# Kernel optimization log

Hardware: AMD Instinct MI355X
Metric: run time of the kernel (lower is better)

## Reference

```python
import jax, jax.numpy as jnp
import numpy as np

N_EMBED = 1024
SEQ_LEN = 2048
BATCH = 4


def setup_inputs() -> dict:
    key = jax.random.key(0)
    ks = jax.random.split(key, 9)
    E = N_EMBED
    x = jax.random.normal(ks[0], (BATCH, SEQ_LEN, E), dtype=jnp.float32)
    s = 0.02
    return {
        "x": x,
        "Wq": jax.random.normal(ks[1], (E, E), dtype=jnp.float32) * s,
        "bq": jnp.zeros((E,), dtype=jnp.float32),
        "Wk": jax.random.normal(ks[2], (E, E), dtype=jnp.float32) * s,
        "bk": jnp.zeros((E,), dtype=jnp.float32),
        "Wv": jax.random.normal(ks[3], (E, E), dtype=jnp.float32) * s,
        "bv": jnp.zeros((E,), dtype=jnp.float32),
        "Wp": jax.random.normal(ks[4], (E, E), dtype=jnp.float32) * s,
        "bp": jnp.zeros((E,), dtype=jnp.float32),
    }


def reference(x, Wq, bq, Wk, bk, Wv, bv, Wp, bp):
    # x: [B, S, E]. Original torch code unpacks (B, C, N) = x.shape and
    # scales by sqrt(C) == sqrt(seq_len)  (a bug we faithfully replicate).
    B, S, E = x.shape
    q = jnp.einsum('bse,fe->bsf', x, Wq) + bq
    k = jnp.einsum('bse,fe->bsf', x, Wk) + bk
    v = jnp.einsum('bse,fe->bsf', x, Wv) + bv
    scale = 1.0 / jnp.sqrt(jnp.asarray(S, dtype=x.dtype))
    scores = jnp.einsum('bqe,bke->bqk', q, k) * scale  # [B, S, S]
    # NOTE: original calls masked_fill (non-inplace) and discards the result,
    # so NO causal mask is actually applied. Replicate that: plain softmax.
    w = jax.nn.softmax(scores, axis=-1)
    o = jnp.einsum('bqk,bke->bqe', w, v)
    out = jnp.einsum('bse,fe->bsf', o, Wp) + bp
    return out
```

## Files before the change

### kernel.cpp

```cpp
#include <hip/hip_runtime.h>


typedef __bf16 bf16x8 __attribute__((ext_vector_type(8)));
typedef float  f32x4  __attribute__((ext_vector_type(4)));
typedef unsigned short u16x8 __attribute__((ext_vector_type(8)));

__device__ __forceinline__ float bf2f(unsigned short u) {
  return __uint_as_float(((unsigned int)u) << 16);
}
__device__ __forceinline__ unsigned short f2bf(float f) {
  unsigned int u = __float_as_uint(f);
  return (unsigned short)((u + 0x7fffu + ((u >> 16) & 1u)) >> 16);
}
__device__ __forceinline__ void gload16(const void* g, void* l) {
  __builtin_amdgcn_global_load_lds(
      (const __attribute__((address_space(1))) void*)g,
      (__attribute__((address_space(3))) void*)l, 16, 0, 0);
}

__global__ __launch_bounds__(256) void cvt_str(
    const float* __restrict__ x, const float* __restrict__ wp,
    unsigned short* __restrict__ x_bf, unsigned short* __restrict__ wp_bf) {
  const float* s;
  unsigned short* d;
  int i;
  if (blockIdx.x < 4096) {
    s = x; d = x_bf; i = (blockIdx.x * 256 + threadIdx.x) * 8;
  } else {
    s = wp; d = wp_bf; i = ((blockIdx.x - 4096) * 256 + threadIdx.x) * 8;
  }
  f32x4 a = *(const f32x4*)(s + i);
  f32x4 b = *(const f32x4*)(s + i + 4);
  u16x8 o;
  o[0] = f2bf(a[0]); o[1] = f2bf(a[1]); o[2] = f2bf(a[2]); o[3] = f2bf(a[3]);
  o[4] = f2bf(b[0]); o[5] = f2bf(b[1]); o[6] = f2bf(b[2]); o[7] = f2bf(b[3]);
  *(u16x8*)(d + i) = o;
}

__global__ __launch_bounds__(256) void cvt_T(
    const float* __restrict__ wq, const float* __restrict__ wk,
    const float* __restrict__ wv, unsigned short* __restrict__ qt,
    unsigned short* __restrict__ kt, unsigned short* __restrict__ vt) {
  const float* in;
  unsigned short* out;
  int b = blockIdx.x;
  if (b < 256)      { in = wq; out = qt; }
  else if (b < 512) { in = wk; out = kt; b -= 256; }
  else              { in = wv; out = vt; b -= 512; }
  const int r0 = (b >> 4) * 64, c0 = (b & 15) * 64;
  __shared__ unsigned short t[64][72];
  const int tid = threadIdx.x;
  const int rr = tid >> 4;
  const int cc4 = (tid & 15) * 4;
#pragma unroll
  for (int p = 0; p < 4; ++p) {
    const int r = rr + p * 16;
    f32x4 v = *(const f32x4*)(in + (size_t)(r0 + r) * 1024 + c0 + cc4);
    t[cc4 + 0][r] = f2bf(v[0]);
    t[cc4 + 1][r] = f2bf(v[1]);
    t[cc4 + 2][r] = f2bf(v[2]);
    t[cc4 + 3][r] = f2bf(v[3]);
  }
  __syncthreads();
  const int wr_ = tid >> 3;
  const int wc8 = (tid & 7) * 8;
#pragma unroll
  for (int p = 0; p < 2; ++p) {
    const int c = wr_ + p * 32;
    u16x8 o;
#pragma unroll
    for (int j = 0; j < 8; ++j) o[j] = t[c][wc8 + j];
    *(u16x8*)(out + (size_t)(c0 + c) * 1024 + r0 + wc8) = o;
  }
}

__global__ __launch_bounds__(256) void cvec(
    const float* __restrict__ bq, const float* __restrict__ Wk,
    const float* __restrict__ Wp, const float* __restrict__ bv,
    float* __restrict__ c1, float* __restrict__ cv, float scale) {
  if (blockIdx.x < 4) {
    const int e = blockIdx.x * 256 + threadIdx.x;
    float acc = 0.f;
    for (int f = 0; f < 1024; ++f) acc += bq[f] * Wk[(size_t)f * 1024 + e];
    c1[e] = acc * scale;
  } else {
    const int e = blockIdx.x - 4;
    float acc = 0.f;
    for (int f = threadIdx.x; f < 1024; f += 256)
      acc += Wp[(size_t)e * 1024 + f] * bv[f];
#pragma unroll
    for (int i = 1; i < 64; i <<= 1) acc += __shfl_xor(acc, i, 64);
    __shared__ float red[4];
    if ((threadIdx.x & 63) == 0) red[threadIdx.x >> 6] = acc;
    __syncthreads();
    if (threadIdx.x == 0) cv[e] = red[0] + red[1] + red[2] + red[3];
  }
}

template <int EPI>
__device__ __forceinline__ void gemm_core(
    char* lds, int nwg, int base,
    const unsigned short* __restrict__ A, const unsigned short* __restrict__ B,
    void* __restrict__ C, const float* __restrict__ bias,
    const float* __restrict__ rowsum,
    int K, long long sA, long long sB, long long sC,
    int nbm, int nbn, int ldc, float scale) {
  char* ldsA = lds;
  char* ldsB = lds + 98304;

  int id = (int)blockIdx.x - base;
  id = (id & 7) * (nwg >> 3) + (id >> 3);
  const int nbmn = nbm * nbn;
  const int bz = id / nbmn;
  const int rem = id - bz * nbmn;
  const int bm = rem / nbn;
  const int bn = rem - bm * nbn;
  const int gm0 = bm * 256, gn0 = bn * 128;

  const unsigned short* Ag = A + (size_t)bz * sA;
  const unsigned short* Bg = B + (size_t)bz * sB;

  const int tid = threadIdx.x;
  const int w = tid >> 6, l = tid & 63;
  const int wr = w >> 1, wc = w & 1;
  const int lr = l & 15;
  const int lk16 = (l >> 4) * 16;
  const int swz = (lr & 7) << 4;

  const int srow = tid >> 3;
  const int sbo  = ((tid & 7) * 16) ^ ((srow & 7) << 4);
  const int sdst = tid * 16;

#define STG_A(region, ktile)                                                   \
  do {                                                                         \
    const char* _b = (const char*)(Ag + (size_t)(gm0 + srow) * K) +            \
                     (size_t)(ktile) * 128 + sbo;                              \
    const size_t _rk = (size_t)64 * K * 2;                                     \
    gload16(_b,           (region) + sdst);                                    \
    gload16(_b + _rk,     (region) + 8192 + sdst);                             \
    gload16(_b + 2 * _rk, (region) + 16384 + sdst);                            \
    gload16(_b + 3 * _rk, (region) + 24576 + sdst);                            \
  } while (0)
#define STG_B(region, ktile)                                                   \
  do {                                                                         \
    const char* _b = (const char*)(Bg + (size_t)(gn0 + srow) * K) +            \
                     (size_t)(ktile) * 128 + sbo;                              \
    const size_t _rk = (size_t)64 * K * 2;                                     \
    gload16(_b,       (region) + sdst);                                        \
    gload16(_b + _rk, (region) + 8192 + sdst);                                 \
  } while (0)

#define RD_A(dst, m, kh)                                                       \
  dst = *(const bf16x8*)(Abuf + (wr * 64 + (m) * 16 + lr) * 128 +              \
                         ((lk16 + (kh) * 64) ^ swz))
#define RD_B(dst, n, kh)                                                       \
  dst = *(const bf16x8*)(Bbuf + (wc * 64 + (n) * 16 + lr) * 128 +              \
                         ((lk16 + (kh) * 64) ^ swz))

#define LGKM_PIN()                                          \
  asm volatile("s_waitcnt lgkmcnt(0)" ::: "memory");        \
  __builtin_amdgcn_sched_barrier(0)

  f32x4 acc[4][4];
#pragma unroll
  for (int i = 0; i < 4; ++i)
#pragma unroll
    for (int j = 0; j < 4; ++j) acc[i][j] = (f32x4){0.f, 0.f, 0.f, 0.f};

  const int nt = K >> 6;

  STG_B(ldsB, 0); STG_A(ldsA, 0);
  if (nt > 1) { STG_B(ldsB + 16384, 1); STG_A(ldsA + 32768, 1); }
  if (nt > 1) { asm volatile("s_waitcnt vmcnt(6)" ::: "memory"); }
  else        { asm volatile("s_waitcnt vmcnt(0)" ::: "memory"); }
  __builtin_amdgcn_s_barrier();

  int cur = 0;
  for (int t = 0; t < nt; ++t) {
    char* Abuf = ldsA + cur * 32768;
    char* Bbuf = ldsB + cur * 16384;
    const int nx2 = (cur + 2 >= 3) ? cur - 1 : cur + 2;
    const bool pf = (t + 2 < nt);

    bf16x8 af[4], bfr[4];
#pragma unroll
    for (int m = 0; m < 4; ++m) RD_A(af[m], m, 0);
#pragma unroll
    for (int n = 0; n < 4; ++n) RD_B(bfr[n], n, 0);
    if (pf) STG_B(ldsB + nx2 * 16384, t + 2);
    __builtin_amdgcn_s_barrier();
    LGKM_PIN();
    __builtin_amdgcn_s_setprio(1);
#pragma unroll
    for (int m = 0; m < 4; ++m)
#pragma unroll
      for (int n = 0; n < 4; ++n)
        acc[m][n] = __builtin_amdgcn_mfma_f32_16x16x32_bf16(af[m], bfr[n],
                                                            acc[m][n], 0, 0, 0);
    __builtin_amdgcn_s_setprio(0);
    __builtin_amdgcn_s_barrier();

#pragma unroll
    for (int m = 0; m < 4; ++m) RD_A(af[m], m, 1);
#pragma unroll
    for (int n = 0; n < 4; ++n) RD_B(bfr[n], n, 1);
    if (pf) STG_A(ldsA + nx2 * 32768, t + 2);
    __builtin_amdgcn_s_barrier();
    LGKM_PIN();
    __builtin_amdgcn_s_setprio(1);
#pragma unroll
    for (int m = 0; m < 4; ++m)
#pragma unroll
      for (int n = 0; n < 4; ++n)
        acc[m][n] = __builtin_amdgcn_mfma_f32_16x16x32_bf16(af[m], bfr[n],
                                                            acc[m][n], 0, 0, 0);
    __builtin_amdgcn_s_setprio(0);
    if (pf)              { asm volatile("s_waitcnt vmcnt(6)" ::: "memory"); }
    else if (t + 1 < nt) { asm volatile("s_waitcnt vmcnt(0)" ::: "memory"); }
    __builtin_amdgcn_s_barrier();

    cur = (cur + 1 >= 3) ? 0 : cur + 1;
  }

  const int cr = (l >> 4) * 4;
  const int cc = l & 15;
#pragma unroll
  for (int m = 0; m < 4; ++m) {
    const int row = gm0 + wr * 64 + m * 16 + cr;
    if constexpr (EPI == 3) {
      const float* rs = rowsum + bz * 2048 + row;
      const f32x4 rv = *(const f32x4*)rs;
      f32x4 inv;
#pragma unroll
      for (int j = 0; j < 4; ++j) inv[j] = 1.0f / rv[j];
      float* Cp = (float*)C + (size_t)bz * sC;
#pragma unroll
      for (int n = 0; n < 4; ++n) {
        const int col = gn0 + wc * 64 + n * 16 + cc;
        const float b = bias[col];
        f32x4 a = acc[m][n];
#pragma unroll
        for (int j = 0; j < 4; ++j)
          Cp[(size_t)(row + j) * ldc + col] = a[j] * inv[j] + b;
      }
    } else {
      unsigned short* Cp = (unsigned short*)C + (size_t)bz * sC;
#pragma unroll
      for (int n = 0; n < 4; ++n) {
        const int col = gn0 + wc * 64 + n * 16 + cc;
        f32x4 a = acc[m][n];
#pragma unroll
        for (int j = 0; j < 4; ++j) {
          float v;
          if constexpr (EPI == 1)      v = a[j] * scale;
          else if constexpr (EPI == 4) v = a[j] + bias[row + j];
          else                         v = a[j] + bias[col];
          Cp[(size_t)(row + j) * ldc + col] = f2bf(v);
        }
      }
    }
  }
#undef STG_A
#undef STG_B
#undef RD_A
#undef RD_B
#undef LGKM_PIN
}

__global__ __launch_bounds__(512) void gweights(
    const unsigned short* WkT, const unsigned short* WqT,
    const unsigned short* Wp, const unsigned short* WvT,
    unsigned short* HT, unsigned short* G, float scale) {
  __shared__ char lds[147456];
  if (blockIdx.x < 32)
    gemm_core<1>(lds, 32, 0, WkT, WqT, HT, nullptr, nullptr,
                 1024, 0, 0, 0, 4, 8, 1024, scale);
  else
    gemm_core<1>(lds, 32, 32, Wp, WvT, G, nullptr, nullptr,
                 1024, 0, 0, 0, 4, 8, 1024, 1.0f);
}
__global__ __launch_bounds__(512) void gr(
    const unsigned short* x, const unsigned short* HT, unsigned short* R,
    const float* c1) {
  __shared__ char lds[147456];
  gemm_core<5>(lds, 256, 0, x, HT, R, c1, nullptr,
               1024, 0, 0, 0, 32, 8, 1024, 0.f);
}
__global__ __launch_bounds__(512) void gvwt(
    const unsigned short* G, const unsigned short* x, unsigned short* VWt,
    const float* cv) {
  __shared__ char lds[147456];
  gemm_core<4>(lds, 256, 0, G, x, VWt, cv, nullptr,
               1024, 0, 2097152, 2097152, 4, 16, 2048, 0.f);
}
__global__ __launch_bounds__(512) void gout(
    const unsigned short* E, const unsigned short* VWt, float* out,
    const float* bp, const float* rowsum) {
  __shared__ char lds[147456];
  gemm_core<3>(lds, 256, 0, E, VWt, out, bp, rowsum,
               2048, 4194304, 2097152, 2097152, 8, 8, 1024, 0.f);
}

__global__ __launch_bounds__(512) void gsco8(
    const unsigned short* __restrict__ A, const unsigned short* __restrict__ B,
    unsigned short* __restrict__ C, float* __restrict__ rowsum,
    int K, long long sA, long long sB, long long sC, int nbm, int nbn) {
  __shared__ char lds[131072];
  char* ldsA = lds;
  char* ldsB = lds + 65536;

  const int nwg = (int)gridDim.x;
  int id = (int)blockIdx.x;
  id = (id & 7) * (nwg >> 3) + (id >> 3);
  const int nbmn = nbm * nbn;
  const int bz = id / nbmn;
  const int rem = id - bz * nbmn;
  const int bm = rem / nbn;
  const int bn = rem - bm * nbn;
  const int gm0 = bm * 256, gn0 = bn * 256;

  const unsigned short* Ag = A + (size_t)bz * sA;
  const unsigned short* Bg = B + (size_t)bz * sB;

  const int tid = threadIdx.x;
  const int w = tid >> 6, l = tid & 63;
  const int wr = w >> 2, wc = w & 3;
  const int lr = l & 15;
  const int lk16 = (l >> 4) * 16;
  const int swz = (lr & 7) << 4;

  const int srow0 = (tid * 16) >> 7;
  const int srow1 = srow0 + 64;
  const int sbo   = ((tid * 16) & 127) ^ ((srow0 & 7) << 4);
  const int sdst0 = tid * 16;
  const int sdst1 = tid * 16 + 8192;

#define STAGE(gbase, grow0, region, ktile)                                     \
  do {                                                                         \
    const char* _s0 =                                                          \
        (const char*)((gbase) + (size_t)((grow0) + srow0) * K) +               \
        (ktile) * 128 + sbo;                                                   \
    const char* _s1 =                                                          \
        (const char*)((gbase) + (size_t)((grow0) + srow1) * K) +               \
        (ktile) * 128 + sbo;                                                   \
    gload16(_s0, (region) + sdst0);                                            \
    gload16(_s1, (region) + sdst1);                                            \
  } while (0)

#define RDA(dst, m, kh) \
  dst = *(const bf16x8*)(Areg + ((m) * 16 + lr) * 128 + ((lk16 + (kh) * 64) ^ swz))
#define RDB(dst, n, kh) \
  dst = *(const bf16x8*)(Breg + (((wc & 1) * 64 + (n) * 16 + lr) * 128) + ((lk16 + (kh) * 64) ^ swz))

  f32x4 acc[8][4];
#pragma unroll
  for (int i = 0; i < 8; ++i)
#pragma unroll
    for (int j = 0; j < 4; ++j) acc[i][j] = (f32x4){0.f, 0.f, 0.f, 0.f};

  bf16x8 af[4][2], bf_[4][2];

#define MM(mi, ai, n)                                                          \
  acc[mi][n] = __builtin_amdgcn_mfma_f32_16x16x32_bf16(af[ai][0], bf_[n][0],   \
                                                       acc[mi][n], 0, 0, 0);   \
  acc[mi][n] = __builtin_amdgcn_mfma_f32_16x16x32_bf16(af[ai][1], bf_[n][1],   \
                                                       acc[mi][n], 0, 0, 0)

#define LGKM_PIN()                                          \
  asm volatile("s_waitcnt lgkmcnt(0)" ::: "memory");        \
  __builtin_amdgcn_sched_barrier(0)

  const int nt = K >> 6;

  STAGE(Bg, gn0,       ldsB + 0,     0);
  STAGE(Bg, gn0 + 128, ldsB + 16384, 0);
  STAGE(Ag, gm0,       ldsA + 0,     0);
  STAGE(Ag, gm0 + 128, ldsA + 16384, 0);
  STAGE(Bg, gn0,       ldsB + 32768,         1);
  STAGE(Bg, gn0 + 128, ldsB + 32768 + 16384, 1);
  STAGE(Ag, gm0,       ldsA + 32768,         1);
  asm volatile("s_waitcnt vmcnt(6)" ::: "memory");
  __builtin_amdgcn_s_barrier();

  for (int t = 0; t < nt; ++t) {
    const int cur = t & 1;
    char* Areg  = ldsA + cur * 32768 + wr * 16384;
    char* Breg  = ldsB + cur * 32768 + (wc >> 1) * 16384;
    char* Anext = ldsA + (cur ^ 1) * 32768;
    char* Acur2 = ldsA + cur * 32768;
    char* Bcur2 = ldsB + cur * 32768;

#pragma unroll
    for (int m = 0; m < 4; ++m) { RDA(af[m][0], m, 0); RDA(af[m][1], m, 1); }
#pragma unroll
    for (int n = 0; n < 2; ++n) { RDB(bf_[n][0], n, 0); RDB(bf_[n][1], n, 1); }
    if (wc < 2) {
#pragma unroll
      for (int n = 2; n < 4; ++n) { RDB(bf_[n][0], n, 0); RDB(bf_[n][1], n, 1); }
    }
    if (t + 1 < nt) STAGE(Ag, gm0 + 128, Anext + 16384, t + 1);
    __builtin_amdgcn_s_barrier();
    LGKM_PIN();
    __builtin_amdgcn_s_setprio(1);
    MM(0, 0, 0); MM(0, 0, 1); MM(1, 1, 0); MM(1, 1, 1);
    MM(2, 2, 0); MM(2, 2, 1); MM(3, 3, 0); MM(3, 3, 1);
    __builtin_amdgcn_s_setprio(0);
    __builtin_amdgcn_s_barrier();

    if (wc >= 2) {
#pragma unroll
      for (int n = 2; n < 4; ++n) { RDB(bf_[n][0], n, 0); RDB(bf_[n][1], n, 1); }
    }
    if (t + 2 < nt) STAGE(Bg, gn0, Bcur2, t + 2);
    __builtin_amdgcn_s_barrier();
    LGKM_PIN();
    __builtin_amdgcn_s_setprio(1);
    MM(0, 0, 2); MM(0, 0, 3); MM(1, 1, 2); MM(1, 1, 3);
    MM(2, 2, 2); MM(2, 2, 3); MM(3, 3, 2); MM(3, 3, 3);
    __builtin_amdgcn_s_setprio(0);
    __builtin_amdgcn_s_barrier();

#pragma unroll
    for (int m = 0; m < 4; ++m) { RDA(af[m][0], m + 4, 0); RDA(af[m][1], m + 4, 1); }
    if (t + 2 < nt) STAGE(Bg, gn0 + 128, Bcur2 + 16384, t + 2);
    __builtin_amdgcn_s_barrier();
    LGKM_PIN();
    __builtin_amdgcn_s_setprio(1);
    MM(4, 0, 0); MM(4, 0, 1); MM(5, 1, 0); MM(5, 1, 1);
    MM(6, 2, 0); MM(6, 2, 1); MM(7, 3, 0); MM(7, 3, 1);
    __builtin_amdgcn_s_setprio(0);
    __builtin_amdgcn_s_barrier();

    if (t + 2 < nt) STAGE(Ag, gm0, Acur2, t + 2);
    __builtin_amdgcn_s_barrier();
    __builtin_amdgcn_s_setprio(1);
    MM(4, 0, 2); MM(4, 0, 3); MM(5, 1, 2); MM(5, 1, 3);
    MM(6, 2, 2); MM(6, 2, 3); MM(7, 3, 2); MM(7, 3, 3);
    __builtin_amdgcn_s_setprio(0);
    if (t + 2 < nt) {
      asm volatile("s_waitcnt vmcnt(6)" ::: "memory");
    } else {
      asm volatile("s_waitcnt vmcnt(0)" ::: "memory");
    }
    __builtin_amdgcn_s_barrier();
  }

  const int cr = (l >> 4) * 4;
  const int cc = l & 15;
  unsigned short* Cp = C + (size_t)bz * sC;
#pragma unroll
  for (int m = 0; m < 8; ++m) {
    const int row = gm0 + wr * 128 + m * 16 + cr;
    float psum[4] = {0.f, 0.f, 0.f, 0.f};
#pragma unroll
    for (int n = 0; n < 4; ++n) {
      const int col = gn0 + wc * 64 + n * 16 + cc;
      f32x4 a = acc[m][n];
#pragma unroll
      for (int j = 0; j < 4; ++j) {
        const unsigned short us = f2bf(__expf(a[j]));
        Cp[(size_t)(row + j) * 2048 + col] = us;
        psum[j] += bf2f(us);
      }
    }
#pragma unroll
    for (int j = 0; j < 4; ++j) {
#pragma unroll
      for (int i = 1; i < 16; i <<= 1) psum[j] += __shfl_xor(psum[j], i, 16);
      if ((l & 15) == 0) atomicAdd(rowsum + bz * 2048 + row + j, psum[j]);
    }
  }
#undef STAGE
#undef RDA
#undef RDB
#undef MM
#undef LGKM_PIN
}

extern "C" void kernel_launch(void* const* d_in, const int* in_sizes, int n_in,
                              void* d_out, int out_size, void* d_ws, size_t ws_size,
                              hipStream_t stream) {
  const float* x  = (const float*)d_in[0];
  const float* Wq = (const float*)d_in[1];
  const float* bq = (const float*)d_in[2];
  const float* Wk = (const float*)d_in[3];
  const float* bk = (const float*)d_in[4];  (void)bk;
  const float* Wv = (const float*)d_in[5];
  const float* bv = (const float*)d_in[6];
  const float* Wp = (const float*)d_in[7];
  const float* bp = (const float*)d_in[8];
  float* out = (float*)d_out;

  char* ws = (char*)d_ws;
  unsigned short* x_bf  = (unsigned short*)(ws);
  unsigned short* Wp_bf = (unsigned short*)(ws + (16ull << 20));
  unsigned short* WqT   = (unsigned short*)(ws + (18ull << 20));
  unsigned short* WkT   = (unsigned short*)(ws + (20ull << 20));
  unsigned short* WvT   = (unsigned short*)(ws + (22ull << 20));
  unsigned short* HT    = (unsigned short*)(ws + (24ull << 20));
  unsigned short* G     = (unsigned short*)(ws + (26ull << 20));
  float*          c1    = (float*)(ws + (28ull << 20));
  float*          cv    = (float*)(ws + (28ull << 20) + 65536);
  unsigned short* R     = (unsigned short*)(ws + (32ull << 20));
  unsigned short* VWt   = (unsigned short*)(ws + (48ull << 20));
  unsigned short* Em    = (unsigned short*)(ws + (64ull << 20));
  float*          rowsum = (float*)(ws + (96ull << 20));

  const float scale = 0.022097086912079608f;

  cvt_str<<<4608, 256, 0, stream>>>(x, Wp, x_bf, Wp_bf);
  cvt_T<<<768, 256, 0, stream>>>(Wq, Wk, Wv, WqT, WkT, WvT);
  cvec<<<1028, 256, 0, stream>>>(bq, Wk, Wp, bv, c1, cv, scale);
  gweights<<<64, 512, 0, stream>>>(WkT, WqT, Wp_bf, WvT, HT, G, scale);
  gr<<<256, 512, 0, stream>>>(x_bf, HT, R, c1);
  gvwt<<<256, 512, 0, stream>>>(G, x_bf, VWt, cv);
  (void)hipMemsetAsync(rowsum, 0, 8192 * sizeof(float), stream);
  gsco8<<<256, 512, 0, stream>>>(R, x_bf, Em, rowsum,
                                 1024, 2097152, 2097152, 4194304, 8, 8);
  gout<<<256, 512, 0, stream>>>(Em, VWt, out, bp, rowsum);
}
```

Before: 188.7 us.

## Merge prep kernels and co-schedule independent GEMMs to cut launches

Collapses the launch sequence from nine operations to five. The weight transposes, Wp conversion and rowsum zeroing now share one kernel. The weight-product GEMMs, x conversion and bias-vector reductions run side by side in a second kernel. The two mid GEMMs (R and VWt) run in one 512-block grid. The aim is to remove launch gaps and small-grid underutilisation, with idle blocks filling in. The risk is load imbalance inside the merged grids, and the high-LDS GEMM blocks share residency with the light blocks.

```diff
diff --git a/kernel.cpp b/kernel.cpp
--- a/kernel.cpp
+++ b/kernel.cpp
@@ -16,85 +16,6 @@
   __builtin_amdgcn_global_load_lds(
       (const __attribute__((address_space(1))) void*)g,
       (__attribute__((address_space(3))) void*)l, 16, 0, 0);
-}
-
-__global__ __launch_bounds__(256) void cvt_str(
-    const float* __restrict__ x, const float* __restrict__ wp,
-    unsigned short* __restrict__ x_bf, unsigned short* __restrict__ wp_bf) {
-  const float* s;
-  unsigned short* d;
-  int i;
-  if (blockIdx.x < 4096) {
-    s = x; d = x_bf; i = (blockIdx.x * 256 + threadIdx.x) * 8;
-  } else {
-    s = wp; d = wp_bf; i = ((blockIdx.x - 4096) * 256 + threadIdx.x) * 8;
-  }
-  f32x4 a = *(const f32x4*)(s + i);
-  f32x4 b = *(const f32x4*)(s + i + 4);
-  u16x8 o;
-  o[0] = f2bf(a[0]); o[1] = f2bf(a[1]); o[2] = f2bf(a[2]); o[3] = f2bf(a[3]);
-  o[4] = f2bf(b[0]); o[5] = f2bf(b[1]); o[6] = f2bf(b[2]); o[7] = f2bf(b[3]);
-  *(u16x8*)(d + i) = o;
-}
-
-__global__ __launch_bounds__(256) void cvt_T(
-    const float* __restrict__ wq, const float* __restrict__ wk,
-    const float* __restrict__ wv, unsigned short* __restrict__ qt,
-    unsigned short* __restrict__ kt, unsigned short* __restrict__ vt) {
-  const float* in;
-  unsigned short* out;
-  int b = blockIdx.x;
-  if (b < 256)      { in = wq; out = qt; }
-  else if (b < 512) { in = wk; out = kt; b -= 256; }
-  else              { in = wv; out = vt; b -= 512; }
-  const int r0 = (b >> 4) * 64, c0 = (b & 15) * 64;
-  __shared__ unsigned short t[64][72];
-  const int tid = threadIdx.x;
-  const int rr = tid >> 4;
-  const int cc4 = (tid & 15) * 4;
-#pragma unroll
-  for (int p = 0; p < 4; ++p) {
-    const int r = rr + p * 16;
-    f32x4 v = *(const f32x4*)(in + (size_t)(r0 + r) * 1024 + c0 + cc4);
-    t[cc4 + 0][r] = f2bf(v[0]);
-    t[cc4 + 1][r] = f2bf(v[1]);
-    t[cc4 + 2][r] = f2bf(v[2]);
-    t[cc4 + 3][r] = f2bf(v[3]);
-  }
-  __syncthreads();
-  const int wr_ = tid >> 3;
-  const int wc8 = (tid & 7) * 8;
-#pragma unroll
-  for (int p = 0; p < 2; ++p) {
-    const int c = wr_ + p * 32;
-    u16x8 o;
-#pragma unroll
-    for (int j = 0; j < 8; ++j) o[j] = t[c][wc8 + j];
-    *(u16x8*)(out + (size_t)(c0 + c) * 1024 + r0 + wc8) = o;
-  }
-}
-
-__global__ __launch_bounds__(256) void cvec(
-    const float* __restrict__ bq, const float* __restrict__ Wk,
-    const float* __restrict__ Wp, const float* __restrict__ bv,
-    float* __restrict__ c1, float* __restrict__ cv, float scale) {
-  if (blockIdx.x < 4) {
-    const int e = blockIdx.x * 256 + threadIdx.x;
-    float acc = 0.f;
-    for (int f = 0; f < 1024; ++f) acc += bq[f] * Wk[(size_t)f * 1024 + e];
-    c1[e] = acc * scale;
-  } else {
-    const int e = blockIdx.x - 4;
-    float acc = 0.f;
-    for (int f = threadIdx.x; f < 1024; f += 256)
-      acc += Wp[(size_t)e * 1024 + f] * bv[f];
-#pragma unroll
-    for (int i = 1; i < 64; i <<= 1) acc += __shfl_xor(acc, i, 64);
-    __shared__ float red[4];
-    if ((threadIdx.x & 63) == 0) red[threadIdx.x >> 6] = acc;
-    __syncthreads();
-    if (threadIdx.x == 0) cv[e] = red[0] + red[1] + red[2] + red[3];
-  }
 }
 
 template <int EPI>
@@ -267,32 +188,119 @@
 #undef LGKM_PIN
 }
 
-__global__ __launch_bounds__(512) void gweights(
-    const unsigned short* WkT, const unsigned short* WqT,
-    const unsigned short* Wp, const unsigned short* WvT,
-    unsigned short* HT, unsigned short* G, float scale) {
+__global__ __launch_bounds__(256) void prep1(
+    const float* __restrict__ wq, const float* __restrict__ wk,
+    const float* __restrict__ wv, const float* __restrict__ wp,
+    unsigned short* __restrict__ qt, unsigned short* __restrict__ kt,
+    unsigned short* __restrict__ vt, unsigned short* __restrict__ wp_bf,
+    float* __restrict__ rowsum) {
+  const int tid = threadIdx.x;
+  if (blockIdx.x >= 1280) {
+    const int i = ((blockIdx.x - 1280) * 256 + tid) * 8;
+    *(f32x4*)(rowsum + i) = (f32x4){0.f, 0.f, 0.f, 0.f};
+    *(f32x4*)(rowsum + i + 4) = (f32x4){0.f, 0.f, 0.f, 0.f};
+    return;
+  }
+  if (blockIdx.x >= 768) {
+    const int i = ((blockIdx.x - 768) * 256 + tid) * 8;
+    f32x4 a = *(const f32x4*)(wp + i);
+    f32x4 b = *(const f32x4*)(wp + i + 4);
+    u16x8 o;
+    o[0] = f2bf(a[0]); o[1] = f2bf(a[1]); o[2] = f2bf(a[2]); o[3] = f2bf(a[3]);
+    o[4] = f2bf(b[0]); o[5] = f2bf(b[1]); o[6] = f2bf(b[2]); o[7] = f2bf(b[3]);
+    *(u16x8*)(wp_bf + i) = o;
+    return;
+  }
+  const float* in;
+  unsigned short* out;
+  int b = blockIdx.x;
+  if (b < 256)      { in = wq; out = qt; }
+  else if (b < 512) { in = wk; out = kt; b -= 256; }
+  else              { in = wv; out = vt; b -= 512; }
+  const int r0 = (b >> 4) * 64, c0 = (b & 15) * 64;
+  __shared__ unsigned short t[64][72];
+  const int rr = tid >> 4;
+  const int cc4 = (tid & 15) * 4;
+#pragma unroll
+  for (int p = 0; p < 4; ++p) {
+    const int r = rr + p * 16;
+    f32x4 v = *(const f32x4*)(in + (size_t)(r0 + r) * 1024 + c0 + cc4);
+    t[cc4 + 0][r] = f2bf(v[0]);
+    t[cc4 + 1][r] = f2bf(v[1]);
+    t[cc4 + 2][r] = f2bf(v[2]);
+    t[cc4 + 3][r] = f2bf(v[3]);
+  }
+  __syncthreads();
+  const int wr_ = tid >> 3;
+  const int wc8 = (tid & 7) * 8;
+#pragma unroll
+  for (int p = 0; p < 2; ++p) {
+    const int c = wr_ + p * 32;
+    u16x8 o;
+#pragma unroll
+    for (int j = 0; j < 8; ++j) o[j] = t[c][wc8 + j];
+    *(u16x8*)(out + (size_t)(c0 + c) * 1024 + r0 + wc8) = o;
+  }
+}
+
+__global__ __launch_bounds__(512) void prep2(
+    const unsigned short* __restrict__ WkT, const unsigned short* __restrict__ WqT,
+    const unsigned short* __restrict__ Wp_bf, const unsigned short* __restrict__ WvT,
+    unsigned short* __restrict__ HT, unsigned short* __restrict__ G,
+    const float* __restrict__ x, unsigned short* __restrict__ x_bf,
+    const float* __restrict__ bq, const float* __restrict__ Wk,
+    const float* __restrict__ Wp, const float* __restrict__ bv,
+    float* __restrict__ c1, float* __restrict__ cv, float scale) {
   __shared__ char lds[147456];
-  if (blockIdx.x < 32)
+  const int bid = (int)blockIdx.x;
+  const int tid = threadIdx.x;
+  if (bid < 32) {
     gemm_core<1>(lds, 32, 0, WkT, WqT, HT, nullptr, nullptr,
                  1024, 0, 0, 0, 4, 8, 1024, scale);
-  else
-    gemm_core<1>(lds, 32, 32, Wp, WvT, G, nullptr, nullptr,
+  } else if (bid < 64) {
+    gemm_core<1>(lds, 32, 32, Wp_bf, WvT, G, nullptr, nullptr,
                  1024, 0, 0, 0, 4, 8, 1024, 1.0f);
-}
-__global__ __launch_bounds__(512) void gr(
+  } else if (bid < 224) {
+    for (int u = (bid - 64) * 512 + tid; u < 1048576; u += 160 * 512) {
+      const int i = u * 8;
+      f32x4 a = *(const f32x4*)(x + i);
+      f32x4 b = *(const f32x4*)(x + i + 4);
+      u16x8 o;
+      o[0] = f2bf(a[0]); o[1] = f2bf(a[1]); o[2] = f2bf(a[2]); o[3] = f2bf(a[3]);
+      o[4] = f2bf(b[0]); o[5] = f2bf(b[1]); o[6] = f2bf(b[2]); o[7] = f2bf(b[3]);
+      *(u16x8*)(x_bf + i) = o;
+    }
+  } else if (bid < 226) {
+    const int e = (bid - 224) * 512 + tid;
+    float acc = 0.f;
+    for (int f = 0; f < 1024; ++f) acc += bq[f] * Wk[(size_t)f * 1024 + e];
+    c1[e] = acc * scale;
+  } else {
+    const int l = tid & 63;
+    for (int e = (bid - 226) * 8 + (tid >> 6); e < 1024; e += 240) {
+      float acc = 0.f;
+#pragma unroll
+      for (int f = l; f < 1024; f += 64) acc += Wp[(size_t)e * 1024 + f] * bv[f];
+#pragma unroll
+      for (int i = 1; i < 64; i <<= 1) acc += __shfl_xor(acc, i, 64);
+      if (l == 0) cv[e] = acc;
+    }
+  }
+}
+
+__global__ __launch_bounds__(512) void gmid(
     const unsigned short* x, const unsigned short* HT, unsigned short* R,
-    const float* c1) {
-  __shared__ char lds[147456];
-  gemm_core<5>(lds, 256, 0, x, HT, R, c1, nullptr,
-               1024, 0, 0, 0, 32, 8, 1024, 0.f);
-}
-__global__ __launch_bounds__(512) void gvwt(
-    const unsigned short* G, const unsigned short* x, unsigned short* VWt,
+    const float* c1, const unsigned short* G, unsigned short* VWt,
     const float* cv) {
   __shared__ char lds[147456];
-  gemm_core<4>(lds, 256, 0, G, x, VWt, cv, nullptr,
-               1024, 0, 2097152, 2097152, 4, 16, 2048, 0.f);
-}
+  if (blockIdx.x < 256)
+    gemm_core<5>(lds, 256, 0, x, HT, R, c1, nullptr,
+                 1024, 0, 0, 0, 32, 8, 1024, 0.f);
+  else
+    gemm_core<4>(lds, 256, 256, G, x, VWt, cv, nullptr,
+                 1024, 0, 2097152, 2097152, 4, 16, 2048, 0.f);
+}
+
 __global__ __launch_bounds__(512) void gout(
     const unsigned short* E, const unsigned short* VWt, float* out,
     const float* bp, const float* rowsum) {
@@ -508,13 +516,10 @@
 
   const float scale = 0.022097086912079608f;
 
-  cvt_str<<<4608, 256, 0, stream>>>(x, Wp, x_bf, Wp_bf);
-  cvt_T<<<768, 256, 0, stream>>>(Wq, Wk, Wv, WqT, WkT, WvT);
-  cvec<<<1028, 256, 0, stream>>>(bq, Wk, Wp, bv, c1, cv, scale);
-  gweights<<<64, 512, 0, stream>>>(WkT, WqT, Wp_bf, WvT, HT, G, scale);
-  gr<<<256, 512, 0, stream>>>(x_bf, HT, R, c1);
-  gvwt<<<256, 512, 0, stream>>>(G, x_bf, VWt, cv);
-  (void)hipMemsetAsync(rowsum, 0, 8192 * sizeof(float), stream);
+  prep1<<<1284, 256, 0, stream>>>(Wq, Wk, Wv, Wp, WqT, WkT, WvT, Wp_bf, rowsum);
+  prep2<<<256, 512, 0, stream>>>(WkT, WqT, Wp_bf, WvT, HT, G,
+                                 x, x_bf, bq, Wk, Wp, bv, c1, cv, scale);
+  gmid<<<512, 512, 0, stream>>>(x_bf, HT, R, c1, G, VWt, cv);
   gsco8<<<256, 512, 0, stream>>>(R, x_bf, Em, rowsum,
                                  1024, 2097152, 2097152, 4194304, 8, 8);
   gout<<<256, 512, 0, stream>>>(Em, VWt, out, bp, rowsum);
```

Result: faster. 169.6 us (-10.1%).
